# Kernel tuning notes

Hardware: AMD Instinct MI355X
Metric: run time of the kernel (lower is better)

## Reference

```python
import jax, jax.numpy as jnp
import numpy as np

S, B, H = 2048, 1, 1024
N_HEADS = 16
HEAD_DIM = H // N_HEADS
E, K, F = 8, 2, 2048  # experts, top_k, ffn_hidden
EPS = 1e-5


def layernorm(x, w, b):
    mu = jnp.mean(x, axis=-1, keepdims=True)
    var = jnp.mean(jnp.square(x - mu), axis=-1, keepdims=True)
    return (x - mu) * jax.lax.rsqrt(var + EPS) * w + b


def setup_inputs() -> dict:
    key = jax.random.key(0)
    ks = jax.random.split(key, 8)
    std = 0.02
    return {
        "x": jax.random.normal(ks[0], (S, B, H), dtype=jnp.float32),
        "ln1_w": jnp.ones((H,), jnp.float32),
        "ln1_b": jnp.zeros((H,), jnp.float32),
        "in_proj_w": jax.random.normal(ks[1], (3 * H, H), jnp.float32) * std,
        "in_proj_b": jnp.zeros((3 * H,), jnp.float32),
        "out_proj_w": jax.random.normal(ks[2], (H, H), jnp.float32) * std,
        "out_proj_b": jnp.zeros((H,), jnp.float32),
        "ln2_w": jnp.ones((H,), jnp.float32),
        "ln2_b": jnp.zeros((H,), jnp.float32),
        "router_w": jax.random.normal(ks[3], (E, H), jnp.float32) * std,
        "w1": jax.random.normal(ks[4], (E, H, F), jnp.float32) * std,
        "w2": jax.random.normal(ks[5], (E, F, H), jnp.float32) * std,
    }


def reference(x, ln1_w, ln1_b, in_proj_w, in_proj_b, out_proj_w, out_proj_b,
              ln2_w, ln2_b, router_w, w1, w2):
    s, b, h = x.shape
    # ---- causal self-attention (nn.MultiheadAttention math) ----
    hn = layernorm(x, ln1_w, ln1_b)
    qkv = hn @ in_proj_w.T + in_proj_b          # [S,B,3H]
    q, k, v = jnp.split(qkv, 3, axis=-1)
    q = q.reshape(s, b, N_HEADS, HEAD_DIM)
    k = k.reshape(s, b, N_HEADS, HEAD_DIM)
    v = v.reshape(s, b, N_HEADS, HEAD_DIM)
    scores = jnp.einsum('sbnd,tbnd->bnst', q, k) / np.sqrt(HEAD_DIM)
    causal = jnp.tril(jnp.ones((s, s), bool))
    scores = jnp.where(causal[None, None], scores, -jnp.inf)
    probs = jax.nn.softmax(scores, axis=-1)
    attn = jnp.einsum('bnst,tbnd->sbnd', probs, v).reshape(s, b, h)
    attn = attn @ out_proj_w.T + out_proj_b
    x1 = x + attn
    # ---- dMoE FFN: router softmax -> top-k gates -> expert GELU MLP ----
    hn2 = layernorm(x1, ln2_w, ln2_b).reshape(s * b, h)   # tokens [T,H]
    logits = hn2 @ router_w.T                              # [T,E]
    rp = jax.nn.softmax(logits, axis=-1)
    topw, topi = jax.lax.top_k(rp, K)                      # [T,K]
    gates = jnp.sum(jax.nn.one_hot(topi, E, dtype=hn2.dtype) * topw[..., None], axis=1)  # [T,E]
    hmid = jax.nn.gelu(jnp.einsum('th,ehf->tef', hn2, w1), approximate=False)  # [T,E,F]
    y = jnp.einsum('tef,efh->th', hmid * gates[:, :, None], w2)                # [T,H]
    return x1 + y.reshape(s, b, h)
```

## Files before the change

kernel.cpp:

```cpp
#include <hip/hip_runtime.h>

#define SL 2048
#define HID 1024
#define NHEAD 16
#define HD 64
#define NEXP 8
#define FF 2048
#define MAXTILE 40
#define MAXROWS (MAXTILE * 128)
#define CPAD 32

typedef short bf16x8 __attribute__((ext_vector_type(8)));
typedef float f32x4 __attribute__((ext_vector_type(4)));
typedef unsigned u32x4 __attribute__((ext_vector_type(4)));

__device__ __forceinline__ unsigned short f2bf(float f) {
  unsigned u = __builtin_bit_cast(unsigned, f);
  u += 0x7fffu + ((u >> 16) & 1u);
  return (unsigned short)(u >> 16);
}

__device__ __forceinline__ void gload16(const void* g, void* l) {
  __builtin_amdgcn_global_load_lds((const __attribute__((address_space(1))) void*)g,
                                   (__attribute__((address_space(3))) void*)l,
                                   16, 0, 0);
}

__device__ __forceinline__ void xcd_remap(int& bx, int& by) {
  const int nx = gridDim.x;
  const int nwg = nx * gridDim.y;
  const int L = by * nx + bx;
  const int per = nwg >> 3;
  const int Lp = (L & 7) * per + (L >> 3);
  bx = Lp % nx;
  by = Lp / nx;
}

#define PIPE_WAIT(i, NT)                                                     \
  if ((i) == (NT) - 1)                                                       \
    asm volatile("s_waitcnt vmcnt(0) lgkmcnt(0)" ::: "memory");              \
  else                                                                       \
    asm volatile("s_waitcnt vmcnt(4) lgkmcnt(0)" ::: "memory");              \
  __builtin_amdgcn_s_barrier();

#define GEMM_FRAGS_MFMA(CC)                                                  \
  bf16x8 af[4], bfr[4];                                                      \
  _Pragma("unroll")                                                          \
  for (int mt = 0; mt < 4; mt++)                                             \
    af[mt] = *reinterpret_cast<const bf16x8*>(                               \
        &Asm[CC][(wm + mt * 16 + la) * 32 + lk]);                            \
  _Pragma("unroll")                                                          \
  for (int nt = 0; nt < 4; nt++)                                             \
    bfr[nt] = *reinterpret_cast<const bf16x8*>(                              \
        &Bsm[CC][(wn + nt * 16 + la) * 32 + lk]);                            \
  __builtin_amdgcn_s_setprio(1);                                             \
  _Pragma("unroll")                                                          \
  for (int mt = 0; mt < 4; mt++)                                             \
    _Pragma("unroll")                                                        \
    for (int nt = 0; nt < 4; nt++)                                           \
      acc[mt][nt] =                                                          \
          __builtin_amdgcn_mfma_f32_16x16x32_bf16(af[mt], bfr[nt], acc[mt][nt], 0, 0, 0); \
  __builtin_amdgcn_s_setprio(0);

#define PIPE_ROT()                                                           \
  cc = (cc == 2) ? 0 : cc + 1;                                               \
  cs = (cs == 2) ? 0 : cs + 1;

__global__ __launch_bounds__(256) void qkv_trans_kernel(
    const unsigned short* __restrict__ A, const unsigned short* __restrict__ Bt,
    const float* __restrict__ bias,
    unsigned short* __restrict__ q_out, unsigned short* __restrict__ k_out,
    unsigned short* __restrict__ vt_out,
    const float* __restrict__ w1, const float* __restrict__ w2,
    unsigned short* __restrict__ w1t, unsigned short* __restrict__ w2t)
{
  __shared__ union {
    struct { unsigned short A[3][4096]; unsigned short B[3][4096]; } g;
    struct { float Afp[64 * 128]; unsigned Bu[128 * 33]; } t;
  } sm;
  const int tid = threadIdx.x;

  if (blockIdx.z == 0) {
    unsigned short (*Asm)[4096] = sm.g.A;
    unsigned short (*Bsm)[4096] = sm.g.B;
    int bx = blockIdx.x, by = blockIdx.y;
    xcd_remap(bx, by);
    const int wave = tid >> 6;
    const int lane = tid & 63;
    const int m0 = by * 128;
    const int n0 = bx * 128;
    const int wm = (wave >> 1) * 64;
    const int wn = (wave & 1) * 64;
    const int la = lane & 15;
    const int lk = (lane >> 4) * 8;

    f32x4 acc[4][4] = {};

    const int srow = tid >> 2;
    const int skoff = (tid & 3) * 8;
    const unsigned short* Ag = A + (size_t)(m0 + srow) * HID + skoff;
    const unsigned short* Bg = Bt + (size_t)(n0 + srow) * HID + skoff;

    auto stage = [&](int s, int k0) {
      gload16(Ag + k0, &Asm[s][wave * 512]);
      gload16(Ag + (size_t)64 * HID + k0, &Asm[s][2048 + wave * 512]);
      gload16(Bg + k0, &Bsm[s][wave * 512]);
      gload16(Bg + (size_t)64 * HID + k0, &Bsm[s][2048 + wave * 512]);
    };

    stage(0, 0);
    stage(1, 32);
    const int NT = HID >> 5;
    int cc = 0, cs = 2;
    for (int i = 0; i < NT; ++i) {
      PIPE_WAIT(i, NT)
      if (i + 2 < NT) stage(cs, (i + 2) << 5);
      GEMM_FRAGS_MFMA(cc)
      PIPE_ROT()
    }

    const int lg = lane >> 4;
#pragma unroll
    for (int mt = 0; mt < 4; mt++) {
#pragma unroll
      for (int nt = 0; nt < 4; nt++) {
#pragma unroll
        for (int r = 0; r < 4; r++) {
          const int row = m0 + wm + mt * 16 + lg * 4 + r;
          const int col = n0 + wn + nt * 16 + la;
          float v = acc[mt][nt][r] + bias[col];
          const int hh = (col & 1023) >> 6;
          const int dd = col & 63;
          const unsigned short bv = f2bf(v);
          if (col < 1024)
            q_out[(size_t)hh * SL * HD + (size_t)row * HD + dd] = bv;
          else if (col < 2048)
            k_out[(size_t)hh * SL * HD + (size_t)row * HD + dd] = bv;
          else
            vt_out[(size_t)hh * HD * SL + (size_t)dd * SL + row] = bv;
        }
      }
    }
  } else {
    const int id = blockIdx.y * 24 + blockIdx.x;
    const int tile = ((int)blockIdx.z - 1) * 384 + id;
    if (tile >= 4096) return;
    const int m = tile >> 8;
    const int t = tile & 255;
    const float* in;
    unsigned short* out;
    int R, C, r0, c0;
    if (m < 8) {
      in = w1 + (size_t)m * HID * FF;  out = w1t + (size_t)m * HID * FF;
      R = HID; C = FF;  r0 = (t >> 4) * 64;  c0 = (t & 15) * 128;
    } else {
      in = w2 + (size_t)(m - 8) * FF * HID;  out = w2t + (size_t)(m - 8) * FF * HID;
      R = FF; C = HID;  r0 = (t >> 3) * 64;  c0 = (t & 7) * 128;
    }
    const int wv = tid >> 6, ln = tid & 63;
#pragma unroll
    for (int p = 0; p < 8; p++) {
      const int ebase = p * 1024 + wv * 256;
      const int eo = ebase + ln * 4;
      const int r = eo >> 7, c = eo & 127;
      gload16(in + (size_t)(r0 + r) * C + c0 + c, (char*)sm.t.Afp + (size_t)ebase * 4);
    }
    asm volatile("s_waitcnt vmcnt(0)" ::: "memory");
    __syncthreads();
#pragma unroll
    for (int it = 0; it < 16; it++) {
      const int idx = it * 256 + tid;
      const int rp = idx >> 7;
      const int c = idx & 127;
      const float v0 = sm.t.Afp[(2 * rp) * 128 + c];
      const float v1 = sm.t.Afp[(2 * rp + 1) * 128 + c];
      sm.t.Bu[c * 33 + rp] = (unsigned)f2bf(v0) | ((unsigned)f2bf(v1) << 16);
    }
    __syncthreads();
#pragma unroll
    for (int it = 0; it < 8; it++) {
      const int idx = it * 256 + tid;
      const int c = idx >> 4;
      const int r4 = (idx & 15) * 4;
      const unsigned u0 = sm.t.Bu[c * 33 + (r4 >> 1)];
      const unsigned u1 = sm.t.Bu[c * 33 + (r4 >> 1) + 1];
      ushort4 u;
      u.x = (unsigned short)(u0 & 0xffff);
      u.y = (unsigned short)(u0 >> 16);
      u.z = (unsigned short)(u1 & 0xffff);
      u.w = (unsigned short)(u1 >> 16);
      *reinterpret_cast<ushort4*>(&out[(size_t)(c0 + c) * R + r0 + r4]) = u;
    }
  }
}

template <int MODE>
__global__ __launch_bounds__(256) void gemm_bt(
    const unsigned short* __restrict__ A, const unsigned short* __restrict__ Bt,
    int M, int N, int Kstride, int Kloop,
    const float* __restrict__ bias,
    float* __restrict__ outf)
{
  __shared__ unsigned short Asm[3][128 * 32];
  __shared__ unsigned short Bsm[3][128 * 32];
  int bx = blockIdx.x, by = blockIdx.y;
  xcd_remap(bx, by);
  const int tid = threadIdx.x;
  const int wave = tid >> 6;
  const int lane = tid & 63;
  const int m0 = by * 128;
  const int n0 = bx * 128;
  const int koff = blockIdx.z * Kloop;
  const int wm = (wave >> 1) * 64;
  const int wn = (wave & 1) * 64;
  const int la = lane & 15;
  const int lk = (lane >> 4) * 8;

  f32x4 acc[4][4] = {};

  const int srow = tid >> 2;
  const int skoff = (tid & 3) * 8;
  const unsigned short* Ag = A + (size_t)(m0 + srow) * Kstride + koff + skoff;
  const unsigned short* Bg = Bt + (size_t)(n0 + srow) * Kstride + koff + skoff;

  auto stage = [&](int s, int k0) {
    gload16(Ag + k0, &Asm[s][wave * 512]);
    gload16(Ag + (size_t)64 * Kstride + k0, &Asm[s][2048 + wave * 512]);
    gload16(Bg + k0, &Bsm[s][wave * 512]);
    gload16(Bg + (size_t)64 * Kstride + k0, &Bsm[s][2048 + wave * 512]);
  };

  stage(0, 0);
  stage(1, 32);
  const int NT = Kloop >> 5;
  int cc = 0, cs = 2;
  for (int i = 0; i < NT; ++i) {
    PIPE_WAIT(i, NT)
    if (i + 2 < NT) stage(cs, (i + 2) << 5);
    GEMM_FRAGS_MFMA(cc)
    PIPE_ROT()
  }

  const int lg = lane >> 4;
#pragma unroll
  for (int mt = 0; mt < 4; mt++) {
#pragma unroll
    for (int nt = 0; nt < 4; nt++) {
#pragma unroll
      for (int r = 0; r < 4; r++) {
        const int row = m0 + wm + mt * 16 + lg * 4 + r;
        const int col = n0 + wn + nt * 16 + la;
        outf[(size_t)blockIdx.z * SL * HID + (size_t)row * HID + col] = acc[mt][nt][r];
      }
    }
  }
}

__global__ __launch_bounds__(256) void gemm_moe1(
    const unsigned short* __restrict__ A, const unsigned short* __restrict__ w1t,
    const int* __restrict__ perm, const float* __restrict__ gateg,
    const int* __restrict__ texp, const int* __restrict__ trow,
    unsigned short* __restrict__ hmidg)
{
  __shared__ unsigned short Asm[3][128 * 32];
  __shared__ unsigned short Bsm[3][128 * 32];
  int bx = blockIdx.x, by = blockIdx.y;
  xcd_remap(bx, by);
  const int e = texp[by];
  if (e < 0) return;
  const int row0 = trow[by];
  const int tid = threadIdx.x;
  const int wave = tid >> 6;
  const int lane = tid & 63;
  const int n0 = bx * 128;
  const int wm = (wave >> 1) * 64;
  const int wn = (wave & 1) * 64;
  const int la = lane & 15;
  const int lk = (lane >> 4) * 8;
  f32x4 acc[4][4] = {};

  const int srow = tid >> 2;
  const int skoff = (tid & 3) * 8;
  const int p0 = perm[row0 + srow];
  const int p1 = perm[row0 + 64 + srow];
  const unsigned short* Ag0 = A + (size_t)(p0 < 0 ? 0 : (p0 >> 1)) * HID + skoff;
  const unsigned short* Ag1 = A + (size_t)(p1 < 0 ? 0 : (p1 >> 1)) * HID + skoff;
  const unsigned short* Bg = w1t + (size_t)e * HID * FF + (size_t)(n0 + srow) * HID + skoff;

  auto stage = [&](int s, int k0) {
    gload16(Ag0 + k0, &Asm[s][wave * 512]);
    gload16(Ag1 + k0, &Asm[s][2048 + wave * 512]);
    gload16(Bg + k0, &Bsm[s][wave * 512]);
    gload16(Bg + (size_t)64 * HID + k0, &Bsm[s][2048 + wave * 512]);
  };

  stage(0, 0);
  stage(1, 32);
  const int NT = HID >> 5;
  int cc = 0, cs = 2;
  for (int i = 0; i < NT; ++i) {
    PIPE_WAIT(i, NT)
    if (i + 2 < NT) stage(cs, (i + 2) << 5);
    GEMM_FRAGS_MFMA(cc)
    PIPE_ROT()
  }

  const int lg = lane >> 4;
#pragma unroll
  for (int mt = 0; mt < 4; mt++) {
    float gr[4];
#pragma unroll
    for (int r = 0; r < 4; r++) gr[r] = gateg[row0 + wm + mt * 16 + lg * 4 + r];
#pragma unroll
    for (int nt = 0; nt < 4; nt++) {
#pragma unroll
      for (int r = 0; r < 4; r++) {
        const int grow = row0 + wm + mt * 16 + lg * 4 + r;
        const int col = n0 + wn + nt * 16 + la;
        const float v = acc[mt][nt][r];
        const float g = 0.5f * v * (1.0f + erff(v * 0.70710678118f));
        hmidg[(size_t)grow * FF + col] = f2bf(g * gr[r]);
      }
    }
  }
}

__global__ __launch_bounds__(256) void gemm_moe2(
    const unsigned short* __restrict__ A, const unsigned short* __restrict__ w2t,
    const int* __restrict__ perm,
    const int* __restrict__ texp, const int* __restrict__ trow,
    float* __restrict__ ybuf)
{
  __shared__ unsigned short Asm[3][128 * 32];
  __shared__ unsigned short Bsm[3][128 * 32];
  int bx = blockIdx.x, by = blockIdx.y;
  xcd_remap(bx, by);
  const int e = texp[by];
  if (e < 0) return;
  const int row0 = trow[by];
  const int tid = threadIdx.x;
  const int wave = tid >> 6;
  const int lane = tid & 63;
  const int n0 = bx * 128;
  const int koff = blockIdx.z * (FF / 2);
  const int wm = (wave >> 1) * 64;
  const int wn = (wave & 1) * 64;
  const int la = lane & 15;
  const int lk = (lane >> 4) * 8;
  f32x4 acc[4][4] = {};

  const int srow = tid >> 2;
  const int skoff = (tid & 3) * 8;
  const unsigned short* Ag = A + (size_t)(row0 + srow) * FF + koff + skoff;
  const unsigned short* Bg = w2t + (size_t)e * FF * HID + (size_t)(n0 + srow) * FF + koff + skoff;

  auto stage = [&](int s, int k0) {
    gload16(Ag + k0, &Asm[s][wave * 512]);
    gload16(Ag + (size_t)64 * FF + k0, &Asm[s][2048 + wave * 512]);
    gload16(Bg + k0, &Bsm[s][wave * 512]);
    gload16(Bg + (size_t)64 * FF + k0, &Bsm[s][2048 + wave * 512]);
  };

  stage(0, 0);
  stage(1, 32);
  const int NT = (FF / 2) >> 5;
  int cc = 0, cs = 2;
  for (int i = 0; i < NT; ++i) {
    PIPE_WAIT(i, NT)
    if (i + 2 < NT) stage(cs, (i + 2) << 5);
    GEMM_FRAGS_MFMA(cc)
    PIPE_ROT()
  }

  const int lg = lane >> 4;
#pragma unroll
  for (int mt = 0; mt < 4; mt++) {
    int pr[4];
#pragma unroll
    for (int r = 0; r < 4; r++) pr[r] = perm[row0 + wm + mt * 16 + lg * 4 + r];
#pragma unroll
    for (int nt = 0; nt < 4; nt++) {
#pragma unroll
      for (int r = 0; r < 4; r++) {
        const int p = pr[r];
        if (p >= 0) {
          const int col = n0 + wn + nt * 16 + la;
          ybuf[(size_t)(blockIdx.z * 2 + (p & 1)) * SL * HID + (size_t)(p >> 1) * HID + col] =
              acc[mt][nt][r];
        }
      }
    }
  }
}

__global__ __launch_bounds__(256) void ln_conv_kernel(
    const float* __restrict__ x, const float* __restrict__ w, const float* __restrict__ b,
    unsigned short* __restrict__ ob,
    const float4* __restrict__ cva, const float4* __restrict__ cvb,
    ushort4* __restrict__ coa, ushort4* __restrict__ cob)
{
  const int tid = threadIdx.x;
  if ((int)blockIdx.x < SL) {
    const int row = blockIdx.x;
    const float4 v = *reinterpret_cast<const float4*>(&x[(size_t)row * HID + tid * 4]);
    float s = v.x + v.y + v.z + v.w;
    float q = v.x * v.x + v.y * v.y + v.z * v.z + v.w * v.w;
    for (int off = 32; off > 0; off >>= 1) {
      s += __shfl_down(s, off);
      q += __shfl_down(q, off);
    }
    __shared__ float ps[4], pq[4];
    const int wave = tid >> 6, lane = tid & 63;
    if (lane == 0) { ps[wave] = s; pq[wave] = q; }
    __syncthreads();
    s = ps[0] + ps[1] + ps[2] + ps[3];
    q = pq[0] + pq[1] + pq[2] + pq[3];
    const float mu = s * (1.0f / HID);
    const float inv = rsqrtf(q * (1.0f / HID) - mu * mu + 1e-5f);
    const int i = tid * 4;
    const float4 wv = *reinterpret_cast<const float4*>(&w[i]);
    const float4 bv = *reinterpret_cast<const float4*>(&b[i]);
    ushort4 u;
    u.x = f2bf((v.x - mu) * inv * wv.x + bv.x);
    u.y = f2bf((v.y - mu) * inv * wv.y + bv.y);
    u.z = f2bf((v.z - mu) * inv * wv.z + bv.z);
    u.w = f2bf((v.w - mu) * inv * wv.w + bv.w);
    *reinterpret_cast<ushort4*>(&ob[(size_t)row * HID + i]) = u;
  } else {
    const int NA = 3 * HID * HID / 4, NB = HID * HID / 4;
    for (int i = ((int)blockIdx.x - SL) * 256 + tid; i < NA + NB; i += 512 * 256) {
      if (i < NA) {
        const float4 v = cva[i];
        ushort4 u; u.x = f2bf(v.x); u.y = f2bf(v.y); u.z = f2bf(v.z); u.w = f2bf(v.w);
        coa[i] = u;
      } else {
        const float4 v = cvb[i - NA];
        ushort4 u; u.x = f2bf(v.x); u.y = f2bf(v.y); u.z = f2bf(v.z); u.w = f2bf(v.w);
        cob[i - NA] = u;
      }
    }
  }
}

__global__ __launch_bounds__(256) void combine_ln(
    const float4* __restrict__ x, const float* __restrict__ bias,
    const float4* __restrict__ p0, const float4* __restrict__ p1,
    float4* __restrict__ x1,
    const float* __restrict__ w, const float* __restrict__ b,
    unsigned short* __restrict__ ob, float* __restrict__ of)
{
  const int row = blockIdx.x;
  const int tid = threadIdx.x;
  const int i4 = row * 256 + tid;
  const int i = tid * 4;
  const float4 bv0 = *reinterpret_cast<const float4*>(&bias[i]);
  const float4 a = x[i4], c = p0[i4], d = p1[i4];
  float4 v;
  v.x = a.x + bv0.x + c.x + d.x;
  v.y = a.y + bv0.y + c.y + d.y;
  v.z = a.z + bv0.z + c.z + d.z;
  v.w = a.w + bv0.w + c.w + d.w;
  x1[i4] = v;
  float s = v.x + v.y + v.z + v.w;
  float q = v.x * v.x + v.y * v.y + v.z * v.z + v.w * v.w;
  for (int off = 32; off > 0; off >>= 1) {
    s += __shfl_down(s, off);
    q += __shfl_down(q, off);
  }
  __shared__ float ps[4], pq[4];
  const int wave = tid >> 6, lane = tid & 63;
  if (lane == 0) { ps[wave] = s; pq[wave] = q; }
  __syncthreads();
  s = ps[0] + ps[1] + ps[2] + ps[3];
  q = pq[0] + pq[1] + pq[2] + pq[3];
  const float mu = s * (1.0f / HID);
  const float inv = rsqrtf(q * (1.0f / HID) - mu * mu + 1e-5f);
  const float4 wv = *reinterpret_cast<const float4*>(&w[i]);
  const float4 bv = *reinterpret_cast<const float4*>(&b[i]);
  const float o0 = (v.x - mu) * inv * wv.x + bv.x;
  const float o1 = (v.y - mu) * inv * wv.y + bv.y;
  const float o2 = (v.z - mu) * inv * wv.z + bv.z;
  const float o3 = (v.w - mu) * inv * wv.w + bv.w;
  ushort4 u; u.x = f2bf(o0); u.y = f2bf(o1); u.z = f2bf(o2); u.w = f2bf(o3);
  *reinterpret_cast<ushort4*>(&ob[(size_t)row * HID + i]) = u;
  float4 o; o.x = o0; o.y = o1; o.z = o2; o.w = o3;
  *reinterpret_cast<float4*>(&of[(size_t)row * HID + i]) = o;
}

__global__ __launch_bounds__(256) void router_kernel(
    const float* __restrict__ hn2f, const float* __restrict__ rw,
    int* __restrict__ ti, float* __restrict__ tg, int* __restrict__ cnt)
{
  __shared__ float wlds[NEXP * HID];
  __shared__ int lcnt[NEXP];
  const int tid = threadIdx.x;
#pragma unroll
  for (int i = 0; i < 8; i++)
    *reinterpret_cast<float4*>(&wlds[i * 1024 + tid * 4]) =
        *reinterpret_cast<const float4*>(&rw[i * 1024 + tid * 4]);
  if (tid < NEXP) lcnt[tid] = 0;
  __syncthreads();

  const int wave = tid >> 6, lane = tid & 63;
#pragma unroll 1
  for (int k = 0; k < 4; k++) {
    const int t = blockIdx.x * 16 + wave * 4 + k;
    float4 xr[4];
#pragma unroll
    for (int c = 0; c < 4; c++)
      xr[c] = *reinterpret_cast<const float4*>(&hn2f[(size_t)t * HID + c * 256 + lane * 4]);
    float p[NEXP];
#pragma unroll
    for (int e = 0; e < NEXP; e++) {
      float s = 0.f;
#pragma unroll
      for (int c = 0; c < 4; c++) {
        const float4 wv = *reinterpret_cast<const float4*>(&wlds[e * 1024 + c * 256 + lane * 4]);
        s += xr[c].x * wv.x + xr[c].y * wv.y + xr[c].z * wv.z + xr[c].w * wv.w;
      }
      s += __shfl_xor(s, 32);
      s += __shfl_xor(s, 16);
      s += __shfl_xor(s, 8);
      s += __shfl_xor(s, 4);
      s += __shfl_xor(s, 2);
      s += __shfl_xor(s, 1);
      p[e] = s;
    }
    if (lane == 0) {
      float mx = p[0];
#pragma unroll
      for (int e = 1; e < NEXP; e++) mx = fmaxf(mx, p[e]);
      float Z = 0.f;
#pragma unroll
      for (int e = 0; e < NEXP; e++) { p[e] = expf(p[e] - mx); Z += p[e]; }
      const float invZ = 1.f / Z;
      int i1 = 0;
#pragma unroll
      for (int e = 1; e < NEXP; e++) if (p[e] > p[i1]) i1 = e;
      int i2 = (i1 == 0) ? 1 : 0;
#pragma unroll
      for (int e = 0; e < NEXP; e++) if (e != i1 && p[e] > p[i2]) i2 = e;
      ti[2 * t] = i1; ti[2 * t + 1] = i2;
      tg[2 * t] = p[i1] * invZ; tg[2 * t + 1] = p[i2] * invZ;
      atomicAdd(&lcnt[i1], 1);
      atomicAdd(&lcnt[i2], 1);
    }
  }
  __syncthreads();
  if (tid < NEXP && lcnt[tid] > 0) atomicAdd(&cnt[tid * CPAD], lcnt[tid]);
}

__global__ void scan_kernel(const int* __restrict__ cnt, int* __restrict__ poff,
                            int* __restrict__ texp, int* __restrict__ trow)
{
  if (threadIdx.x == 0 && blockIdx.x == 0) {
    int off = 0, nt = 0;
    for (int e = 0; e < NEXP; e++) {
      poff[e] = off;
      const int c = cnt[e * CPAD];
      const int ntl = (c + 127) >> 7;
      for (int i = 0; i < ntl; i++) { texp[nt] = e; trow[nt] = off + i * 128; nt++; }
      off += ntl * 128;
    }
    for (int i = nt; i < MAXTILE; i++) { texp[i] = -1; trow[i] = 0; }
  }
}

__global__ __launch_bounds__(256) void build_kernel(
    const int* __restrict__ ti, const float* __restrict__ tg,
    const int* __restrict__ poff, int* __restrict__ fill,
    int* __restrict__ perm, float* __restrict__ gateg)
{
  __shared__ int lcnt[NEXP], lbase[NEXP];
  const int tid = threadIdx.x;
  if (tid < NEXP) lcnt[tid] = 0;
  __syncthreads();
  const int t = blockIdx.x * 256 + tid;
  int e0 = ti[2 * t], e1 = ti[2 * t + 1];
  int l0 = atomicAdd(&lcnt[e0], 1);
  int l1 = atomicAdd(&lcnt[e1], 1);
  __syncthreads();
  if (tid < NEXP) lbase[tid] = (lcnt[tid] > 0) ? atomicAdd(&fill[tid * CPAD], lcnt[tid]) : 0;
  __syncthreads();
  int pos0 = poff[e0] + lbase[e0] + l0;
  int pos1 = poff[e1] + lbase[e1] + l1;
  perm[pos0] = 2 * t;
  gateg[pos0] = tg[2 * t];
  perm[pos1] = 2 * t + 1;
  gateg[pos1] = tg[2 * t + 1];
}

__global__ __launch_bounds__(256) void final_add(
    const float4* __restrict__ x1, const float4* __restrict__ y0,
    const float4* __restrict__ y1, const float4* __restrict__ y2,
    const float4* __restrict__ y3, float4* __restrict__ out)
{
  const int i = blockIdx.x * 256 + threadIdx.x;
  const float4 a = x1[i], b = y0[i], c = y1[i], d = y2[i], e = y3[i];
  float4 o;
  o.x = a.x + b.x + c.x + d.x + e.x;
  o.y = a.y + b.y + c.y + d.y + e.y;
  o.z = a.z + b.z + c.z + d.z + e.z;
  o.w = a.w + b.w + c.w + d.w + e.w;
  out[i] = o;
}

#define SC2 0.1803368801111204f
#define PPITCH 20
__global__ __launch_bounds__(512) void attn_kernel(
    const unsigned short* __restrict__ qb, const unsigned short* __restrict__ kb,
    const unsigned short* __restrict__ vtb, unsigned short* __restrict__ attn)
{
  const int h = blockIdx.y;
  const int tid = threadIdx.x;
  const int wave = tid >> 6, lane = tid & 63;
  const int grp = wave >> 2;
  const int w4 = wave & 3;
  const int la = lane & 15, lg = lane >> 4;
  const int la7 = la & 7;
  __shared__ unsigned short Kt[2][2][64 * 64];
  __shared__ unsigned short Vt[2][2][64 * 64];
  __shared__ unsigned plds[8 * 32 * PPITCH];
  const unsigned short* qh = qb + (size_t)h * SL * HD;
  const unsigned short* kh = kb + (size_t)h * SL * HD;
  const unsigned short* vh = vtb + (size_t)h * HD * SL;
  unsigned* pu = &plds[wave * 32 * PPITCH];

  const int sr_lo = w4 * 8 + (lane >> 3);
  const int ss = lane & 7;

  auto stageKV = [&](int t, int buf) {
    const int kvb = t * 64;
#pragma unroll
    for (int j = 0; j < 2; j++) {
      const int row = j * 32 + sr_lo;
      const int s = ss ^ (row & 7);
      gload16(kh + (size_t)(kvb + row) * HD + s * 8, &Kt[grp][buf][j * 2048 + w4 * 512]);
      gload16(vh + (size_t)row * SL + kvb + s * 8, &Vt[grp][buf][j * 2048 + w4 * 512]);
    }
  };

  for (int half = 0; half < 2; half++) {
    const int qt = half ? (31 - blockIdx.x) : blockIdx.x;
    const int m0 = qt * 64 + w4 * 16;
    const int T = qt + 1;
    const int S = (T + 1) >> 1;
    const int q = m0 + la;

    bf16x8 aq0 = *reinterpret_cast<const bf16x8*>(&qh[(size_t)(m0 + la) * HD + lg * 8]);
    bf16x8 aq1 = *reinterpret_cast<const bf16x8*>(&qh[(size_t)(m0 + la) * HD + 32 + lg * 8]);

    f32x4 oacc[4] = {};
    float mrun = -1e30f, lrun = 0.f;

    if (grp < T) stageKV(grp, 0);
    __syncthreads();
    int cur = 0;

    for (int s = 0; s < S; s++) {
      const int tmy = 2 * s + grp;
      if (tmy + 2 < T) stageKV(tmy + 2, cur ^ 1);
      if (tmy < T) {
        const int kv0 = tmy * 64;
        const unsigned short* Kb = Kt[grp][cur];
        const unsigned short* Vb = Vt[grp][cur];

        f32x4 sac[4] = {};
        __builtin_amdgcn_s_setprio(1);
#pragma unroll
        for (int nt = 0; nt < 4; nt++) {
          const int row = nt * 16 + la;
          bf16x8 b0 = *reinterpret_cast<const bf16x8*>(&Kb[row * 64 + ((lg ^ la7) << 3)]);
          bf16x8 b1 = *reinterpret_cast<const bf16x8*>(&Kb[row * 64 + (((4 + lg) ^ la7) << 3)]);
          sac[nt] = __builtin_amdgcn_mfma_f32_16x16x32_bf16(b0, aq0, sac[nt], 0, 0, 0);
          sac[nt] = __builtin_amdgcn_mfma_f32_16x16x32_bf16(b1, aq1, sac[nt], 0, 0, 0);
        }
        __builtin_amdgcn_s_setprio(0);
        float sv[4][4];
        const bool diag = (tmy == qt);
#pragma unroll
        for (int nt = 0; nt < 4; nt++)
#pragma unroll
          for (int r = 0; r < 4; r++) {
            float xs = sac[nt][r] * SC2;
            if (diag && (kv0 + nt * 16 + lg * 4 + r) > q) xs = -1e30f;
            sv[nt][r] = xs;
          }
        float pm = fmaxf(fmaxf(sv[0][0], sv[0][1]), fmaxf(sv[0][2], sv[0][3]));
#pragma unroll
        for (int nt = 1; nt < 4; nt++)
          pm = fmaxf(pm, fmaxf(fmaxf(sv[nt][0], sv[nt][1]), fmaxf(sv[nt][2], sv[nt][3])));
        pm = fmaxf(pm, __shfl_xor(pm, 16));
        pm = fmaxf(pm, __shfl_xor(pm, 32));
        const float mn = fmaxf(mrun, pm);
        float rs = 0.f;
#pragma unroll
        for (int nt = 0; nt < 4; nt++)
#pragma unroll
          for (int r = 0; r < 4; r++) {
            const float pe = exp2f(sv[nt][r] - mn);
            sv[nt][r] = pe;
            rs += pe;
          }
        rs += __shfl_xor(rs, 16);
        rs += __shfl_xor(rs, 32);
        if (__ballot(pm > mrun) != 0ULL) {
          const float al = exp2f(mrun - mn);
#pragma unroll
          for (int dt = 0; dt < 4; dt++)
#pragma unroll
            for (int r = 0; r < 4; r++) oacc[dt][r] *= al;
          lrun = lrun * al + rs;
          mrun = mn;
        } else {
          lrun += rs;
        }
#pragma unroll
        for (int nt = 0; nt < 4; nt++)
#pragma unroll
          for (int rp = 0; rp < 2; rp++) {
            unsigned pk;
            asm("v_cvt_pk_bf16_f32 %0, %1, %2"
                : "=v"(pk) : "v"(sv[nt][rp * 2]), "v"(sv[nt][rp * 2 + 1]));
            pu[(nt * 8 + lg * 2 + rp) * PPITCH + la] = pk;
          }
        asm volatile("s_waitcnt lgkmcnt(0)" ::: "memory");
        __builtin_amdgcn_sched_barrier(0);
        u32x4 w0, w1;
#pragma unroll
        for (int jj = 0; jj < 4; jj++) {
          w0[jj] = pu[(lg * 4 + jj) * PPITCH + la];
          w1[jj] = pu[(16 + lg * 4 + jj) * PPITCH + la];
        }
        const bf16x8 pa0 = __builtin_bit_cast(bf16x8, w0);
        const bf16x8 pa1 = __builtin_bit_cast(bf16x8, w1);
        __builtin_amdgcn_s_setprio(1);
#pragma unroll
        for (int dt = 0; dt < 4; dt++) {
          const int row = dt * 16 + la;
          bf16x8 v0 = *reinterpret_cast<const bf16x8*>(&Vb[row * 64 + ((lg ^ la7) << 3)]);
          bf16x8 v1 = *reinterpret_cast<const bf16x8*>(&Vb[row * 64 + (((4 + lg) ^ la7) << 3)]);
          oacc[dt] = __builtin_amdgcn_mfma_f32_16x16x32_bf16(v0, pa0, oacc[dt], 0, 0, 0);
          oacc[dt] = __builtin_amdgcn_mfma_f32_16x16x32_bf16(v1, pa1, oacc[dt], 0, 0, 0);
        }
        __builtin_amdgcn_s_setprio(0);
      }
      __syncthreads();
      cur ^= 1;
    }

    float* xb = (float*)&Kt[0][0][0];
    float* mlb = (float*)&Vt[0][0][0];
    if (grp == 1) {
#pragma unroll
      for (int dt = 0; dt < 4; dt++)
#pragma unroll
        for (int r = 0; r < 4; r++)
          xb[w4 * 1024 + (dt * 16 + lg * 4 + r) * 16 + la] = oacc[dt][r];
      if (lg == 0) {
        mlb[w4 * 32 + la * 2] = mrun;
        mlb[w4 * 32 + la * 2 + 1] = lrun;
      }
    }
    __syncthreads();
    if (grp == 0) {
      const float m1 = mlb[w4 * 32 + la * 2];
      const float l1 = mlb[w4 * 32 + la * 2 + 1];
      const float mm = fmaxf(mrun, m1);
      const float a0 = exp2f(mrun - mm);
      const float a1 = exp2f(m1 - mm);
      const float linv = 1.0f / (lrun * a0 + l1 * a1);
#pragma unroll
      for (int dt = 0; dt < 4; dt++) {
        ushort4 u;
        float o0 = (oacc[dt][0] * a0 + xb[w4 * 1024 + (dt * 16 + lg * 4 + 0) * 16 + la] * a1) * linv;
        float o1 = (oacc[dt][1] * a0 + xb[w4 * 1024 + (dt * 16 + lg * 4 + 1) * 16 + la] * a1) * linv;
        float o2 = (oacc[dt][2] * a0 + xb[w4 * 1024 + (dt * 16 + lg * 4 + 2) * 16 + la] * a1) * linv;
        float o3 = (oacc[dt][3] * a0 + xb[w4 * 1024 + (dt * 16 + lg * 4 + 3) * 16 + la] * a1) * linv;
        u.x = f2bf(o0); u.y = f2bf(o1); u.z = f2bf(o2); u.w = f2bf(o3);
        *reinterpret_cast<ushort4*>(&attn[(size_t)q * HID + h * HD + dt * 16 + lg * 4]) = u;
      }
    }
    __syncthreads();
  }
}

extern "C" void kernel_launch(void* const* d_in, const int* in_sizes, int n_in,
                              void* d_out, int out_size, void* d_ws, size_t ws_size,
                              hipStream_t stream)
{
  const float* x          = (const float*)d_in[0];
  const float* ln1_w      = (const float*)d_in[1];
  const float* ln1_b      = (const float*)d_in[2];
  const float* in_proj_w  = (const float*)d_in[3];
  const float* in_proj_b  = (const float*)d_in[4];
  const float* out_proj_w = (const float*)d_in[5];
  const float* out_proj_b = (const float*)d_in[6];
  const float* ln2_w      = (const float*)d_in[7];
  const float* ln2_b      = (const float*)d_in[8];
  const float* router_w   = (const float*)d_in[9];
  const float* w1         = (const float*)d_in[10];
  const float* w2         = (const float*)d_in[11];
  float* out = (float*)d_out;

  char* ws = (char*)d_ws;
  size_t off = 0;
  auto alloc = [&](size_t bytes) -> void* {
    void* p = ws + off;
    off += (bytes + 255) & ~(size_t)255;
    return p;
  };
  unsigned short* hn_b   = (unsigned short*)alloc((size_t)SL * HID * 2);
  unsigned short* ipw_b  = (unsigned short*)alloc((size_t)3 * HID * HID * 2);
  unsigned short* opw_b  = (unsigned short*)alloc((size_t)HID * HID * 2);
  unsigned short* qb     = (unsigned short*)alloc((size_t)SL * HID * 2);
  unsigned short* kb     = (unsigned short*)alloc((size_t)SL * HID * 2);
  unsigned short* vtb    = (unsigned short*)alloc((size_t)SL * HID * 2);
  unsigned short* attn_b = (unsigned short*)alloc((size_t)SL * HID * 2);
  float*          x1     = (float*)alloc((size_t)SL * HID * 4);
  float*          pbuf   = (float*)alloc((size_t)2 * SL * HID * 4);
  unsigned short* hn2_b  = (unsigned short*)alloc((size_t)SL * HID * 2);
  float*          hn2_f  = (float*)alloc((size_t)SL * HID * 4);
  unsigned short* w1t    = (unsigned short*)alloc((size_t)NEXP * HID * FF * 2);
  unsigned short* w2t    = (unsigned short*)alloc((size_t)NEXP * HID * FF * 2);
  unsigned short* hmidg  = (unsigned short*)alloc((size_t)MAXROWS * FF * 2);
  float*          ybuf   = (float*)alloc((size_t)4 * SL * HID * 4);
  int*            ti     = (int*)alloc((size_t)SL * 2 * 4);
  float*          tg     = (float*)alloc((size_t)SL * 2 * 4);
  int*            perm   = (int*)alloc((size_t)MAXROWS * 4);
  float*          gateg  = (float*)alloc((size_t)MAXROWS * 4);
  int*            cnt    = (int*)alloc(NEXP * CPAD * 4);
  int*            fill   = (int*)alloc(NEXP * CPAD * 4);
  int*            poff   = (int*)alloc(64 * 4);
  int*            texp   = (int*)alloc(64 * 4);
  int*            trow   = (int*)alloc(64 * 4);

  const dim3 blk(256);

  hipMemsetAsync(cnt, 0, NEXP * CPAD * 4, stream);
  hipMemsetAsync(fill, 0, NEXP * CPAD * 4, stream);
  hipMemsetAsync(perm, 0xFF, (size_t)MAXROWS * 4, stream);
  hipMemsetAsync(gateg, 0, (size_t)MAXROWS * 4, stream);

  ln_conv_kernel<<<SL + 512, blk, 0, stream>>>(
      x, ln1_w, ln1_b, hn_b,
      (const float4*)in_proj_w, (const float4*)out_proj_w,
      (ushort4*)ipw_b, (ushort4*)opw_b);

  qkv_trans_kernel<<<dim3(3 * HID / 128, SL / 128, 12), blk, 0, stream>>>(
      hn_b, ipw_b, in_proj_b, qb, kb, vtb, w1, w2, w1t, w2t);

  attn_kernel<<<dim3(16, NHEAD), dim3(512), 0, stream>>>(qb, kb, vtb, attn_b);

  gemm_bt<2><<<dim3(HID / 128, SL / 128, 2), blk, 0, stream>>>(
      attn_b, opw_b, SL, HID, HID, HID / 2,
      out_proj_b, pbuf);

  combine_ln<<<SL, blk, 0, stream>>>(
      (const float4*)x, out_proj_b, (const float4*)pbuf,
      (const float4*)(pbuf + (size_t)SL * HID), (float4*)x1,
      ln2_w, ln2_b, hn2_b, hn2_f);

  router_kernel<<<SL / 16, blk, 0, stream>>>(hn2_f, router_w, ti, tg, cnt);
  scan_kernel<<<1, 64, 0, stream>>>(cnt, poff, texp, trow);
  build_kernel<<<SL / 256, blk, 0, stream>>>(ti, tg, poff, fill, perm, gateg);

  gemm_moe1<<<dim3(FF / 128, MAXTILE), blk, 0, stream>>>(
      hn2_b, w1t, perm, gateg, texp, trow, hmidg);
  gemm_moe2<<<dim3(HID / 128, MAXTILE, 2), blk, 0, stream>>>(
      hmidg, w2t, perm, texp, trow, ybuf);

  final_add<<<SL * HID / 1024, blk, 0, stream>>>(
      (const float4*)x1, (const float4*)ybuf,
      (const float4*)(ybuf + (size_t)SL * HID),
      (const float4*)(ybuf + (size_t)2 * SL * HID),
      (const float4*)(ybuf + (size_t)3 * SL * HID),
      (float4*)out);
}
```

Baseline: 251.4 us.

## Spread MoE weight transpose tiles across LN, QKV and out-proj kernels

The fp32-to-bf16 transpose of the expert weights w1/w2 (4096 tiles) used to run entirely as extra blocks of the QKV GEMM kernel. It is now split three ways: 512 tiles go to extra blocks of the layernorm/convert kernel, 2688 stay in the QKV kernel, and 896 go to extra z-slices of the out-projection GEMM, which is specialised with constant strides. The aim is to fill idle CUs in the smaller kernels and shorten the QKV kernel's tail. The cost is larger LDS unions in the LN kernel and the out-proj GEMM, which may reduce their occupancy, plus more bandwidth contention inside those kernels.

Result: no change. 250.3 us (-0.4%).

```diff
diff --git a/kernel.cpp b/kernel.cpp
--- a/kernel.cpp
+++ b/kernel.cpp
@@ -34,6 +34,61 @@
   const int Lp = (L & 7) * per + (L >> 3);
   bx = Lp % nx;
   by = Lp / nx;
+}
+
+struct TransLds { float Afp[64 * 128]; unsigned Bu[128 * 33]; };
+
+__device__ __forceinline__ void trans_tile(
+    int tile, const float* __restrict__ w1, const float* __restrict__ w2,
+    unsigned short* __restrict__ w1t, unsigned short* __restrict__ w2t,
+    int tid, TransLds* T)
+{
+  const int m = tile >> 8;
+  const int t = tile & 255;
+  const float* in;
+  unsigned short* out;
+  int R, C, r0, c0;
+  if (m < 8) {
+    in = w1 + (size_t)m * HID * FF;  out = w1t + (size_t)m * HID * FF;
+    R = HID; C = FF;  r0 = (t >> 4) * 64;  c0 = (t & 15) * 128;
+  } else {
+    in = w2 + (size_t)(m - 8) * FF * HID;  out = w2t + (size_t)(m - 8) * FF * HID;
+    R = FF; C = HID;  r0 = (t >> 3) * 64;  c0 = (t & 7) * 128;
+  }
+  const int wv = tid >> 6, ln = tid & 63;
+#pragma unroll
+  for (int p = 0; p < 8; p++) {
+    const int ebase = p * 1024 + wv * 256;
+    const int eo = ebase + ln * 4;
+    const int r = eo >> 7, c = eo & 127;
+    gload16(in + (size_t)(r0 + r) * C + c0 + c, (char*)T->Afp + (size_t)ebase * 4);
+  }
+  asm volatile("s_waitcnt vmcnt(0)" ::: "memory");
+  __syncthreads();
+#pragma unroll
+  for (int it = 0; it < 16; it++) {
+    const int idx = it * 256 + tid;
+    const int rp = idx >> 7;
+    const int c = idx & 127;
+    const float v0 = T->Afp[(2 * rp) * 128 + c];
+    const float v1 = T->Afp[(2 * rp + 1) * 128 + c];
+    T->Bu[c * 33 + rp] = (unsigned)f2bf(v0) | ((unsigned)f2bf(v1) << 16);
+  }
+  __syncthreads();
+#pragma unroll
+  for (int it = 0; it < 8; it++) {
+    const int idx = it * 256 + tid;
+    const int c = idx >> 4;
+    const int r4 = (idx & 15) * 4;
+    const unsigned u0 = T->Bu[c * 33 + (r4 >> 1)];
+    const unsigned u1 = T->Bu[c * 33 + (r4 >> 1) + 1];
+    ushort4 u;
+    u.x = (unsigned short)(u0 & 0xffff);
+    u.y = (unsigned short)(u0 >> 16);
+    u.z = (unsigned short)(u1 & 0xffff);
+    u.w = (unsigned short)(u1 >> 16);
+    *reinterpret_cast<ushort4*>(&out[(size_t)(c0 + c) * R + r0 + r4]) = u;
+  }
 }
 
 #define PIPE_WAIT(i, NT)                                                     \
@@ -76,7 +131,7 @@
 {
   __shared__ union {
     struct { unsigned short A[3][4096]; unsigned short B[3][4096]; } g;
-    struct { float Afp[64 * 128]; unsigned Bu[128 * 33]; } t;
+    TransLds t;
   } sm;
   const int tid = threadIdx.x;
 
@@ -143,74 +198,39 @@
     }
   } else {
     const int id = blockIdx.y * 24 + blockIdx.x;
-    const int tile = ((int)blockIdx.z - 1) * 384 + id;
-    if (tile >= 4096) return;
-    const int m = tile >> 8;
-    const int t = tile & 255;
-    const float* in;
-    unsigned short* out;
-    int R, C, r0, c0;
-    if (m < 8) {
-      in = w1 + (size_t)m * HID * FF;  out = w1t + (size_t)m * HID * FF;
-      R = HID; C = FF;  r0 = (t >> 4) * 64;  c0 = (t & 15) * 128;
-    } else {
-      in = w2 + (size_t)(m - 8) * FF * HID;  out = w2t + (size_t)(m - 8) * FF * HID;
-      R = FF; C = HID;  r0 = (t >> 3) * 64;  c0 = (t & 7) * 128;
-    }
-    const int wv = tid >> 6, ln = tid & 63;
-#pragma unroll
-    for (int p = 0; p < 8; p++) {
-      const int ebase = p * 1024 + wv * 256;
-      const int eo = ebase + ln * 4;
-      const int r = eo >> 7, c = eo & 127;
-      gload16(in + (size_t)(r0 + r) * C + c0 + c, (char*)sm.t.Afp + (size_t)ebase * 4);
-    }
-    asm volatile("s_waitcnt vmcnt(0)" ::: "memory");
-    __syncthreads();
-#pragma unroll
-    for (int it = 0; it < 16; it++) {
-      const int idx = it * 256 + tid;
-      const int rp = idx >> 7;
-      const int c = idx & 127;
-      const float v0 = sm.t.Afp[(2 * rp) * 128 + c];
-      const float v1 = sm.t.Afp[(2 * rp + 1) * 128 + c];
-      sm.t.Bu[c * 33 + rp] = (unsigned)f2bf(v0) | ((unsigned)f2bf(v1) << 16);
-    }
-    __syncthreads();
-#pragma unroll
-    for (int it = 0; it < 8; it++) {
-      const int idx = it * 256 + tid;
-      const int c = idx >> 4;
-      const int r4 = (idx & 15) * 4;
-      const unsigned u0 = sm.t.Bu[c * 33 + (r4 >> 1)];
-      const unsigned u1 = sm.t.Bu[c * 33 + (r4 >> 1) + 1];
-      ushort4 u;
-      u.x = (unsigned short)(u0 & 0xffff);
-      u.y = (unsigned short)(u0 >> 16);
-      u.z = (unsigned short)(u1 & 0xffff);
-      u.w = (unsigned short)(u1 >> 16);
-      *reinterpret_cast<ushort4*>(&out[(size_t)(c0 + c) * R + r0 + r4]) = u;
-    }
-  }
-}
-
-template <int MODE>
-__global__ __launch_bounds__(256) void gemm_bt(
+    const int tile = 512 + ((int)blockIdx.z - 1) * 384 + id;
+    trans_tile(tile, w1, w2, w1t, w2t, tid, &sm.t);
+  }
+}
+
+__global__ __launch_bounds__(256) void gemm_bt2(
     const unsigned short* __restrict__ A, const unsigned short* __restrict__ Bt,
-    int M, int N, int Kstride, int Kloop,
-    const float* __restrict__ bias,
-    float* __restrict__ outf)
-{
-  __shared__ unsigned short Asm[3][128 * 32];
-  __shared__ unsigned short Bsm[3][128 * 32];
+    float* __restrict__ outf,
+    const float* __restrict__ w1, const float* __restrict__ w2,
+    unsigned short* __restrict__ w1t, unsigned short* __restrict__ w2t)
+{
+  __shared__ union {
+    struct { unsigned short A[3][4096]; unsigned short B[3][4096]; } g;
+    TransLds t;
+  } sm;
+  const int tid = threadIdx.x;
+
+  if (blockIdx.z >= 2) {
+    const int id = blockIdx.y * 8 + blockIdx.x;
+    const int tile = 3200 + ((int)blockIdx.z - 2) * 128 + id;
+    trans_tile(tile, w1, w2, w1t, w2t, tid, &sm.t);
+    return;
+  }
+
+  unsigned short (*Asm)[4096] = sm.g.A;
+  unsigned short (*Bsm)[4096] = sm.g.B;
   int bx = blockIdx.x, by = blockIdx.y;
   xcd_remap(bx, by);
-  const int tid = threadIdx.x;
   const int wave = tid >> 6;
   const int lane = tid & 63;
   const int m0 = by * 128;
   const int n0 = bx * 128;
-  const int koff = blockIdx.z * Kloop;
+  const int koff = blockIdx.z * (HID / 2);
   const int wm = (wave >> 1) * 64;
   const int wn = (wave & 1) * 64;
   const int la = lane & 15;
@@ -220,19 +240,19 @@
 
   const int srow = tid >> 2;
   const int skoff = (tid & 3) * 8;
-  const unsigned short* Ag = A + (size_t)(m0 + srow) * Kstride + koff + skoff;
-  const unsigned short* Bg = Bt + (size_t)(n0 + srow) * Kstride + koff + skoff;
+  const unsigned short* Ag = A + (size_t)(m0 + srow) * HID + koff + skoff;
+  const unsigned short* Bg = Bt + (size_t)(n0 + srow) * HID + koff + skoff;
 
   auto stage = [&](int s, int k0) {
     gload16(Ag + k0, &Asm[s][wave * 512]);
-    gload16(Ag + (size_t)64 * Kstride + k0, &Asm[s][2048 + wave * 512]);
+    gload16(Ag + (size_t)64 * HID + k0, &Asm[s][2048 + wave * 512]);
     gload16(Bg + k0, &Bsm[s][wave * 512]);
-    gload16(Bg + (size_t)64 * Kstride + k0, &Bsm[s][2048 + wave * 512]);
+    gload16(Bg + (size_t)64 * HID + k0, &Bsm[s][2048 + wave * 512]);
   };
 
   stage(0, 0);
   stage(1, 32);
-  const int NT = Kloop >> 5;
+  const int NT = (HID / 2) >> 5;
   int cc = 0, cs = 2;
   for (int i = 0; i < NT; ++i) {
     PIPE_WAIT(i, NT)
@@ -397,8 +417,11 @@
     const float* __restrict__ x, const float* __restrict__ w, const float* __restrict__ b,
     unsigned short* __restrict__ ob,
     const float4* __restrict__ cva, const float4* __restrict__ cvb,
-    ushort4* __restrict__ coa, ushort4* __restrict__ cob)
-{
+    ushort4* __restrict__ coa, ushort4* __restrict__ cob,
+    const float* __restrict__ w1, const float* __restrict__ w2,
+    unsigned short* __restrict__ w1t, unsigned short* __restrict__ w2t)
+{
+  __shared__ union { struct { float ps[4], pq[4]; } l; TransLds t; } sm;
   const int tid = threadIdx.x;
   if ((int)blockIdx.x < SL) {
     const int row = blockIdx.x;
@@ -409,12 +432,11 @@
       s += __shfl_down(s, off);
       q += __shfl_down(q, off);
     }
-    __shared__ float ps[4], pq[4];
     const int wave = tid >> 6, lane = tid & 63;
-    if (lane == 0) { ps[wave] = s; pq[wave] = q; }
+    if (lane == 0) { sm.l.ps[wave] = s; sm.l.pq[wave] = q; }
     __syncthreads();
-    s = ps[0] + ps[1] + ps[2] + ps[3];
-    q = pq[0] + pq[1] + pq[2] + pq[3];
+    s = sm.l.ps[0] + sm.l.ps[1] + sm.l.ps[2] + sm.l.ps[3];
+    q = sm.l.pq[0] + sm.l.pq[1] + sm.l.pq[2] + sm.l.pq[3];
     const float mu = s * (1.0f / HID);
     const float inv = rsqrtf(q * (1.0f / HID) - mu * mu + 1e-5f);
     const int i = tid * 4;
@@ -426,7 +448,7 @@
     u.z = f2bf((v.z - mu) * inv * wv.z + bv.z);
     u.w = f2bf((v.w - mu) * inv * wv.w + bv.w);
     *reinterpret_cast<ushort4*>(&ob[(size_t)row * HID + i]) = u;
-  } else {
+  } else if ((int)blockIdx.x < SL + 512) {
     const int NA = 3 * HID * HID / 4, NB = HID * HID / 4;
     for (int i = ((int)blockIdx.x - SL) * 256 + tid; i < NA + NB; i += 512 * 256) {
       if (i < NA) {
@@ -439,6 +461,9 @@
         cob[i - NA] = u;
       }
     }
+  } else {
+    const int tile = (int)blockIdx.x - SL - 512;
+    trans_tile(tile, w1, w2, w1t, w2t, tid, &sm.t);
   }
 }
 
@@ -842,19 +867,19 @@
   hipMemsetAsync(perm, 0xFF, (size_t)MAXROWS * 4, stream);
   hipMemsetAsync(gateg, 0, (size_t)MAXROWS * 4, stream);
 
-  ln_conv_kernel<<<SL + 512, blk, 0, stream>>>(
+  ln_conv_kernel<<<SL + 1024, blk, 0, stream>>>(
       x, ln1_w, ln1_b, hn_b,
       (const float4*)in_proj_w, (const float4*)out_proj_w,
-      (ushort4*)ipw_b, (ushort4*)opw_b);
-
-  qkv_trans_kernel<<<dim3(3 * HID / 128, SL / 128, 12), blk, 0, stream>>>(
+      (ushort4*)ipw_b, (ushort4*)opw_b,
+      w1, w2, w1t, w2t);
+
+  qkv_trans_kernel<<<dim3(3 * HID / 128, SL / 128, 8), blk, 0, stream>>>(
       hn_b, ipw_b, in_proj_b, qb, kb, vtb, w1, w2, w1t, w2t);
 
   attn_kernel<<<dim3(16, NHEAD), dim3(512), 0, stream>>>(qb, kb, vtb, attn_b);
 
-  gemm_bt<2><<<dim3(HID / 128, SL / 128, 2), blk, 0, stream>>>(
-      attn_b, opw_b, SL, HID, HID, HID / 2,
-      out_proj_b, pbuf);
+  gemm_bt2<<<dim3(HID / 128, SL / 128, 9), blk, 0, stream>>>(
+      attn_b, opw_b, pbuf, w1, w2, w1t, w2t);
 
   combine_ln<<<SL, blk, 0, stream>>>(
       (const float4*)x, out_proj_b, (const float4*)pbuf,
```
